# Kernel tuning notes

Measured on AMD Instinct MI355X. Metric: run time of the kernel, lower is better.

## Reference

```python
import jax, jax.numpy as jnp
import numpy as np

PATCH = 14

def _patchify(t, p):
    # (B,C,H,W) -> (B*pH*pW, C, p*p)
    B, C, H, W = t.shape
    pH, pW = H // p, W // p
    t = t.reshape(B, C, pH, p, pW, p).transpose(0, 2, 4, 1, 3, 5)
    return t.reshape(B * pH * pW, C, p * p)

def _unpatchify(t, B, C, H, W, p):
    pH, pW = H // p, W // p
    t = t.reshape(B, pH, pW, C, p, p).transpose(0, 3, 1, 4, 2, 5)
    return t.reshape(B, C, H, W)

def setup_inputs() -> dict:
    key = jax.random.key(0)
    ks = jax.random.split(key, 9)
    B, C, H, W = 4, 256, 224, 224
    s = 1.0 / np.sqrt(C)
    return {
        "x": jax.random.normal(ks[0], (B, C, H, W), jnp.float32),
        "skip0": jax.random.normal(ks[1], (B, C, 112, 112), jnp.float32),
        "skip1": jax.random.normal(ks[2], (B, C, 56, 56), jnp.float32),
        "Wq": jax.random.normal(ks[3], (C, C), jnp.float32) * s,
        "bq": jax.random.normal(ks[4], (C,), jnp.float32) * 0.01,
        "Wk": jax.random.normal(ks[5], (C, C), jnp.float32) * s,
        "bk": jax.random.normal(ks[6], (C,), jnp.float32) * 0.01,
        "Wv": jax.random.normal(ks[7], (C, C), jnp.float32) * s,
        "bv": jax.random.normal(ks[8], (C,), jnp.float32) * 0.01,
    }

def reference(x, skip0, skip1, Wq, bq, Wk, bk, Wv, bv):
    B, C, H, W = x.shape
    p = PATCH
    xp = _patchify(x, p)                       # (N, C, L), L = p*p
    # 1x1 conv on x (query) is shared across skips
    Q = jnp.einsum('oc,ncl->nol', Wq, xp) + bq[None, :, None]
    out = 0.0
    for skip in (skip0, skip1):
        sk = jax.image.resize(skip, (B, C, H, W), method='bilinear')  # align_corners=False
        sp = _patchify(sk, p)
        K = jnp.einsum('oc,ncl->nol', Wk, sp) + bk[None, :, None]
        V = jnp.einsum('oc,ncl->nol', Wv, sp) + bv[None, :, None]
        attn = jax.nn.softmax(jnp.einsum('ncl,ncm->nlm', Q, K), axis=-1)  # unscaled, per original
        out = out + jnp.einsum('nlm,ncm->ncl', attn, V)
    return _unpatchify(out, B, C, H, W, p)
```

## Files before the change

### kernel.cpp

```cpp
#include <hip/hip_runtime.h>

typedef _Float16 f16;
typedef _Float16 f16x8 __attribute__((ext_vector_type(8)));
typedef float f32x4 __attribute__((ext_vector_type(4)));

#define DEV static __device__ __forceinline__

constexpr int  NPATCH = 1024;
constexpr int  LLEN   = 196;
constexpr long NLROWS = (long)NPATCH * LLEN;

DEV void g2l16(const void* g, void* l) {
  __builtin_amdgcn_global_load_lds(
      (const __attribute__((address_space(1))) unsigned int*)g,
      (__attribute__((address_space(3))) unsigned int*)l, 16, 0, 0);
}

DEV unsigned pk2(float a, float b) {
  union { f16 h[2]; unsigned u; } z;
  z.h[0] = (f16)a; z.h[1] = (f16)b;
  return z.u;
}

__global__ __launch_bounds__(256) void k0_prep(
    const float* __restrict__ Wq, const float* __restrict__ Wk,
    const float* __restrict__ Wv, const float* __restrict__ bq,
    f16* __restrict__ G16, f16* __restrict__ Wv16, float* __restrict__ u32) {
  int bx = blockIdx.x, t = threadIdx.x;
  if (bx < 256) {
    int c = bx;
    float acc = 0.f;
    for (int o = 0; o < 256; ++o) acc += Wq[o*256 + c] * Wk[o*256 + t];
    G16[c*256 + t] = (f16)acc;
  } else if (bx == 256) {
    float acc = 0.f;
    for (int o = 0; o < 256; ++o) acc += bq[o] * Wk[o*256 + t];
    u32[t] = acc;
  } else {
    for (int r = 0; r < 256; ++r) Wv16[r*256 + t] = (f16)Wv[r*256 + t];
  }
}

__global__ __launch_bounds__(256) void k1_pack(
    const float* __restrict__ src, int Hs, int Ws, float invS,
    f16* __restrict__ dst, float* __restrict__ ub4,
    const float* __restrict__ u32, int do_ub) {
  __shared__ unsigned tile[32 * 225];
  __shared__ float us[64];
  int bx = blockIdx.x;
  int cc0 = (bx & 3) * 64;
  int bi = bx >> 2;
  int i  = bi % 14; bi /= 14;
  int py = bi & 15; int b = bi >> 4;
  int y = py*14 + i;
  int t = threadIdx.x;
  if (t < 64) us[t] = u32[cc0 + t];

  if (invS == 1.0f) {
    int xh = t & 7, pr = t >> 3;
    const float* b0 = src + ((long)(b*256 + cc0 + 2*pr)) * 50176 + y*224;
    const float* b1 = b0 + 50176;
#pragma unroll
    for (int it = 0; it < 7; ++it) {
      int x0 = (it*8 + xh) * 4;
      float4 va = *(const float4*)(b0 + x0);
      float4 vb = *(const float4*)(b1 + x0);
      tile[pr*225 + x0 + 0] = pk2(va.x, vb.x);
      tile[pr*225 + x0 + 1] = pk2(va.y, vb.y);
      tile[pr*225 + x0 + 2] = pk2(va.z, vb.z);
      tile[pr*225 + x0 + 3] = pk2(va.w, vb.w);
    }
  } else {
    float fy  = (y + 0.5f) * invS - 0.5f;
    float y0f = floorf(fy);
    float wy1 = fy - y0f, wy0 = 1.f - wy1;
    int y0 = (int)y0f, y1 = (int)y0f + 1;
    y0 = min(max(y0, 0), Hs-1); y1 = min(max(y1, 0), Hs-1);
    long plane = (long)Hs * Ws;
    int xl = t & 63, c4 = t >> 6;
    for (int xp = 0; xp < 4; ++xp) {
      int x = xp*64 + xl;
      if (x < 224) {
        float fx  = (x + 0.5f) * invS - 0.5f;
        float x0f = floorf(fx);
        float wx1 = fx - x0f, wx0 = 1.f - wx1;
        int x0 = (int)x0f, x1 = (int)x0f + 1;
        x0 = min(max(x0, 0), Ws-1); x1 = min(max(x1, 0), Ws-1);
        int o00 = y0*Ws + x0, o01 = y0*Ws + x1;
        int o10 = y1*Ws + x0, o11 = y1*Ws + x1;
#pragma unroll
        for (int pp = 0; pp < 8; ++pp) {
          int pr = c4*8 + pp;
          const float* base0 = src + ((long)(b*256 + cc0 + 2*pr)) * plane;
          const float* base1 = base0 + plane;
          float va = wy0*(wx0*base0[o00] + wx1*base0[o01])
                   + wy1*(wx0*base0[o10] + wx1*base0[o11]);
          float vb = wy0*(wx0*base1[o00] + wx1*base1[o01])
                   + wy1*(wx0*base1[o10] + wx1*base1[o11]);
          tile[pr*225 + x] = pk2(va, vb);
        }
      }
    }
  }
  __syncthreads();
  int q = t & 7, xg = t >> 3;
  float4 u0, u1;
  if (do_ub) {
    u0 = *(const float4*)(us + q*8);
    u1 = *(const float4*)(us + q*8 + 4);
  }
  for (int xo = 0; xo < 7; ++xo) {
    int x = xo*32 + xg;
    unsigned p0 = tile[(q*4+0)*225 + x];
    unsigned p1 = tile[(q*4+1)*225 + x];
    unsigned p2 = tile[(q*4+2)*225 + x];
    unsigned p3 = tile[(q*4+3)*225 + x];
    int px = x / 14, j = x % 14;
    int m = i*14 + j;
    long nm = (long)(b*256 + py*16 + px) * 196 + m;
    uint4 w; w.x = p0; w.y = p1; w.z = p2; w.w = p3;
    *reinterpret_cast<uint4*>(dst + nm*256 + cc0 + q*8) = w;
    if (do_ub) {
      union { unsigned u; f16 h[2]; } c0, c1, c2, c3;
      c0.u = p0; c1.u = p1; c2.u = p2; c3.u = p3;
      float part = u0.x*(float)c0.h[0] + u0.y*(float)c0.h[1]
                 + u0.z*(float)c1.h[0] + u0.w*(float)c1.h[1]
                 + u1.x*(float)c2.h[0] + u1.y*(float)c2.h[1]
                 + u1.z*(float)c3.h[0] + u1.w*(float)c3.h[1];
      part += __shfl_xor(part, 1);
      part += __shfl_xor(part, 2);
      part += __shfl_xor(part, 4);
      if (q == 0) ub4[(long)(bx & 3) * NLROWS + nm] = part;
    }
  }
}

__global__ __launch_bounds__(256) void k2_kv(
    const f16* __restrict__ SPT, const f16* __restrict__ G16,
    const f16* __restrict__ Wv16, f16* __restrict__ KtT, f16* __restrict__ VT2) {
  __shared__ __align__(16) char ldsA[64 * 80];
  __shared__ __align__(16) char ldsB[512 * 80];
  int tid = threadIdx.x;
  int lane = tid & 63, wv = tid >> 6;
  long nm0 = (long)blockIdx.x * 64;
  f32x4 zero = {0.f, 0.f, 0.f, 0.f};
  f32x4 acc[4][8];
#pragma unroll
  for (int a = 0; a < 4; ++a)
#pragma unroll
    for (int bb = 0; bb < 8; ++bb) acc[a][bb] = zero;
  int col0 = wv * 128;
  int r15 = lane & 15, quad = lane >> 4;
  for (int k0 = 0; k0 < 256; k0 += 32) {
    __syncthreads();
#pragma unroll
    for (int call = 0; call < 2; ++call) {
      int slot = call*256 + tid;
      if (slot < 320) {
        int row = slot / 5, part = slot % 5;
        int pp_ = part < 4 ? part : 0;
        g2l16(SPT + ((nm0 + row)*256 + k0 + pp_*8), ldsA + slot*16);
      }
    }
#pragma unroll
    for (int call = 0; call < 10; ++call) {
      int slot = call*256 + tid;
      int row = slot / 5, part = slot % 5;
      int pp_ = part < 4 ? part : 0;
      const f16* g = (row < 256) ? (G16 + (row*256 + k0 + pp_*8))
                                 : (Wv16 + ((row - 256)*256 + k0 + pp_*8));
      g2l16(g, ldsB + slot*16);
    }
    __syncthreads();
    f16x8 af[4];
#pragma unroll
    for (int rt = 0; rt < 4; ++rt)
      af[rt] = *(const f16x8*)(ldsA + (rt*16 + r15)*80 + quad*16);
#pragma unroll
    for (int tc = 0; tc < 8; ++tc) {
      f16x8 bf = *(const f16x8*)(ldsB + (col0 + tc*16 + r15)*80 + quad*16);
#pragma unroll
      for (int rt = 0; rt < 4; ++rt)
        acc[rt][tc] = __builtin_amdgcn_mfma_f32_16x16x32_f16(af[rt], bf, acc[rt][tc], 0, 0, 0);
    }
  }
  __syncthreads();
  f16* ldsV = (f16*)ldsB;
  if (wv >= 2) {
#pragma unroll
    for (int rt = 0; rt < 4; ++rt)
#pragma unroll
      for (int tc = 0; tc < 8; ++tc) {
        int o = col0 - 256 + tc*16 + r15;
#pragma unroll
        for (int reg = 0; reg < 4; ++reg) {
          int row = rt*16 + quad*4 + reg;
          ldsV[row*258 + o] = (f16)acc[rt][tc][reg];
        }
      }
  } else {
#pragma unroll
    for (int rt = 0; rt < 4; ++rt)
#pragma unroll
      for (int tc = 0; tc < 8; ++tc) {
        int colc = col0 + tc*16 + r15;
#pragma unroll
        for (int reg = 0; reg < 4; ++reg) {
          long row = nm0 + rt*16 + quad*4 + reg;
          KtT[row*256 + colc] = (f16)acc[rt][tc][reg];
        }
      }
  }
  __syncthreads();
  {
    int row = tid & 63;
    long nm = nm0 + row;
    int n = (int)(nm / 196), m = (int)(nm % 196);
    long vbase = ((long)n * 256) * 224 + m;
    int o0 = (tid >> 6) * 64;
    for (int it = 0; it < 64; ++it) {
      int o = o0 + it;
      VT2[vbase + (long)o * 224] = ldsV[row*258 + o];
    }
  }
}

__global__ __launch_bounds__(256) void k3_s(
    const f16* __restrict__ XT, const f16* __restrict__ KtT,
    const float* __restrict__ ub, f16* __restrict__ Pout) {
  __shared__ __align__(16) char ldsA[64 * 144];
  __shared__ __align__(16) char ldsB[208 * 144];
  __shared__ float ubs[208];
  int tid = threadIdx.x;
  int lane = tid & 63, wv = tid >> 6;
  int bx = blockIdx.x;
  int n  = ((bx >> 5) << 3) | (bx & 7);
  int l0 = ((bx >> 3) & 3) * 64;
  long base = (long)n * 196;
  for (int s = tid; s < 208; s += 256) {
    float v = 0.f;
    if (s < 196) {
      long o = base + s;
      v = ub[o] + ub[NLROWS + o] + ub[2*NLROWS + o] + ub[3*NLROWS + o];
    }
    ubs[s] = v;
  }
  f32x4 zero = {0.f, 0.f, 0.f, 0.f};
  f32x4 acc[13];
#pragma unroll
  for (int t = 0; t < 13; ++t) acc[t] = zero;
  int r15 = lane & 15, quad = lane >> 4;
  for (int k0 = 0; k0 < 256; k0 += 64) {
    __syncthreads();
#pragma unroll
    for (int call = 0; call < 3; ++call) {
      int slot = call*256 + tid;
      if (slot < 576) {
        int row = slot / 9, part = slot % 9;
        int pp_ = part < 8 ? part : 0;
        int l = l0 + row; l = l > 195 ? 195 : l;
        g2l16(XT + ((base + l)*256 + k0 + pp_*8), ldsA + slot*16);
      }
    }
#pragma unroll
    for (int call = 0; call < 8; ++call) {
      int slot = call*256 + tid;
      if (slot < 1872) {
        int row = slot / 9, part = slot % 9;
        int pp_ = part < 8 ? part : 0;
        int m = row > 195 ? 195 : row;
        g2l16(KtT + ((base + m)*256 + k0 + pp_*8), ldsB + slot*16);
      }
    }
    __syncthreads();
#pragma unroll
    for (int ks = 0; ks < 2; ++ks) {
      f16x8 af = *(const f16x8*)(ldsA + (wv*16 + r15)*144 + (ks*4 + quad)*16);
#pragma unroll
      for (int t = 0; t < 13; ++t) {
        f16x8 bf = *(const f16x8*)(ldsB + (t*16 + r15)*144 + (ks*4 + quad)*16);
        acc[t] = __builtin_amdgcn_mfma_f32_16x16x32_f16(af, bf, acc[t], 0, 0, 0);
      }
    }
  }
  float mx[4] = {-1e30f, -1e30f, -1e30f, -1e30f};
#pragma unroll
  for (int t = 0; t < 13; ++t) {
    int colb = t*16 + r15;
    float ubv = ubs[colb];
    bool valid = colb < 196;
#pragma unroll
    for (int reg = 0; reg < 4; ++reg) {
      float v = acc[t][reg] + ubv;
      acc[t][reg] = v;
      if (valid) mx[reg] = fmaxf(mx[reg], v);
    }
  }
#pragma unroll
  for (int reg = 0; reg < 4; ++reg) {
    float m = mx[reg];
    m = fmaxf(m, __shfl_xor(m, 1));
    m = fmaxf(m, __shfl_xor(m, 2));
    m = fmaxf(m, __shfl_xor(m, 4));
    m = fmaxf(m, __shfl_xor(m, 8));
    mx[reg] = m;
  }
  float sum[4] = {0.f, 0.f, 0.f, 0.f};
#pragma unroll
  for (int t = 0; t < 13; ++t) {
    int colb = t*16 + r15;
    bool valid = colb < 196;
#pragma unroll
    for (int reg = 0; reg < 4; ++reg) {
      float p = valid ? __expf(acc[t][reg] - mx[reg]) : 0.f;
      acc[t][reg] = p;
      sum[reg] += p;
    }
  }
#pragma unroll
  for (int reg = 0; reg < 4; ++reg) {
    float s = sum[reg];
    s += __shfl_xor(s, 1);
    s += __shfl_xor(s, 2);
    s += __shfl_xor(s, 4);
    s += __shfl_xor(s, 8);
    sum[reg] = 1.0f / s;
  }
#pragma unroll
  for (int reg = 0; reg < 4; ++reg) {
    int l = l0 + wv*16 + quad*4 + reg;
    if (l < 196) {
      long prow = (base + l) * 224;
#pragma unroll
      for (int t = 0; t < 13; ++t)
        Pout[prow + t*16 + r15] = (f16)(acc[t][reg] * sum[reg]);
      Pout[prow + 208 + r15] = (f16)0.f;
    }
  }
}

__global__ __launch_bounds__(256) void k4_o(
    const f16* __restrict__ Pbuf, const f16* __restrict__ VT2,
    f16* __restrict__ Obuf, int mode) {
  __shared__ __align__(16) char ldsA[2][64 * 80];
  __shared__ __align__(16) char ldsB[2][256 * 80];
  int tid = threadIdx.x;
  int lane = tid & 63, wv = tid >> 6;
  int bx = blockIdx.x;
  int n  = ((bx >> 5) << 3) | (bx & 7);
  int l0 = ((bx >> 3) & 3) * 64;
  f32x4 zero = {0.f, 0.f, 0.f, 0.f};
  f32x4 acc[16];
#pragma unroll
  for (int t = 0; t < 16; ++t) acc[t] = zero;
  int r15 = lane & 15, quad = lane >> 4;

  auto stage = [&](int buf, int m0) {
#pragma unroll
    for (int call = 0; call < 2; ++call) {
      int slot = call*256 + tid;
      if (slot < 320) {
        int row = slot / 5, part = slot % 5;
        int pp_ = part < 4 ? part : 0;
        long nl = (long)n*196 + l0 + row;
        if (nl > NLROWS - 1) nl = NLROWS - 1;
        g2l16(Pbuf + (nl*224 + m0 + pp_*8), ldsA[buf] + slot*16);
      }
    }
#pragma unroll
    for (int call = 0; call < 5; ++call) {
      int slot = call*256 + tid;
      int row = slot / 5, part = slot % 5;
      int pp_ = part < 4 ? part : 0;
      g2l16(VT2 + (((long)(n*256 + row))*224 + m0 + pp_*8), ldsB[buf] + slot*16);
    }
  };

  stage(0, 0);
  __syncthreads();
  for (int it = 0; it < 7; ++it) {
    int cur = it & 1;
    if (it < 6) stage(cur ^ 1, 32*(it+1));
    f16x8 af = *(const f16x8*)(ldsA[cur] + (wv*16 + r15)*80 + quad*16);
#pragma unroll
    for (int t = 0; t < 16; ++t) {
      f16x8 bf = *(const f16x8*)(ldsB[cur] + (t*16 + r15)*80 + quad*16);
      acc[t] = __builtin_amdgcn_mfma_f32_16x16x32_f16(af, bf, acc[t], 0, 0, 0);
    }
    __syncthreads();
  }
#pragma unroll
  for (int reg = 0; reg < 4; ++reg) {
    int l = l0 + wv*16 + quad*4 + reg;
    if (l < 196) {
      long orow = ((long)n*196 + l) * 256;
#pragma unroll
      for (int t = 0; t < 16; ++t) {
        int c = t*16 + r15;
        float v = acc[t][reg];
        if (mode == 0) Obuf[orow + c] = (f16)v;
        else           Obuf[orow + c] = (f16)(v + (float)Obuf[orow + c]);
      }
    }
  }
}

__global__ __launch_bounds__(256) void k5_unpatch(
    const f16* __restrict__ Obuf, const float* __restrict__ bv,
    float* __restrict__ out) {
  __shared__ float lds[64 * 225];
  int bx = blockIdx.x;
  int cc = (bx & 3) * 64;  bx >>= 2;
  int i  = bx % 14; bx /= 14;
  int py = bx & 15; int b = bx >> 4;
  int t = threadIdx.x;
  int cl = t & 63, pg = t >> 6;
  for (int it = 0; it < 56; ++it) {
    int pr = it*4 + pg;
    int px = pr / 14, j = pr % 14;
    int n = b*256 + py*16 + px;
    float v = (float)Obuf[((long)n*196 + i*14 + j)*256 + cc + cl];
    lds[cl*225 + px*14 + j] = v;
  }
  __syncthreads();
  int yy = py*14 + i;
  for (int c = 0; c < 64; ++c) {
    float bb = 2.0f * bv[cc + c];
    if (t < 224)
      out[(((long)(b*256 + cc + c))*224 + yy)*224 + t] = lds[c*225 + t] + bb;
  }
}

extern "C" void kernel_launch(void* const* d_in, const int* in_sizes, int n_in,
                              void* d_out, int out_size, void* d_ws, size_t ws_size,
                              hipStream_t stream) {
  (void)in_sizes; (void)n_in; (void)out_size; (void)ws_size;
  const float* x     = (const float*)d_in[0];
  const float* skip0 = (const float*)d_in[1];
  const float* skip1 = (const float*)d_in[2];
  const float* Wq    = (const float*)d_in[3];
  const float* bq    = (const float*)d_in[4];
  const float* Wk    = (const float*)d_in[5];
  const float* Wv    = (const float*)d_in[7];
  const float* bv    = (const float*)d_in[8];
  float* out = (float*)d_out;

  char* ws = (char*)d_ws;
  size_t off = 0;
  auto alloc = [&](size_t bytes) {
    char* p = ws + off;
    off += (bytes + 255) & ~(size_t)255;
    return p;
  };
  f16*   XT   = (f16*)  alloc((size_t)NLROWS * 256 * 2);
  f16*   SPT  = (f16*)  alloc((size_t)NLROWS * 256 * 2);
  f16*   KtT  = (f16*)  alloc((size_t)NLROWS * 256 * 2);
  f16*   VT2  = (f16*)  alloc((size_t)NPATCH * 256 * 224 * 2);
  f16*   Obuf = (f16*)  alloc((size_t)NLROWS * 256 * 2);
  float* ub   = (float*)alloc((size_t)NLROWS * 4 * 4);
  f16*   G16  = (f16*)  alloc(256 * 256 * 2);
  f16*   Wv16 = (f16*)  alloc(256 * 256 * 2);
  float* u32  = (float*)alloc(256 * 4);
  f16*   P    = SPT;

  k0_prep<<<258, 256, 0, stream>>>(Wq, Wk, Wv, bq, G16, Wv16, u32);
  k1_pack<<<3584, 256, 0, stream>>>(x, 224, 224, 1.0f, XT, nullptr, u32, 0);

  const float* skips[2] = {skip0, skip1};
  int   hs[2]   = {112, 56};
  float invs[2] = {0.5f, 0.25f};
  for (int s = 0; s < 2; ++s) {
    k1_pack<<<3584, 256, 0, stream>>>(skips[s], hs[s], hs[s], invs[s], SPT, ub, u32, 1);
    k2_kv<<<3136, 256, 0, stream>>>(SPT, G16, Wv16, KtT, VT2);
    k3_s <<<4096, 256, 0, stream>>>(XT, KtT, ub, P);
    k4_o <<<4096, 256, 0, stream>>>(P, VT2, Obuf, s);
  }
  k5_unpatch<<<3584, 256, 0, stream>>>(Obuf, bv, out);
}
```

Baseline: 1.709 ms.

## Fuse score-softmax and PV kernels to keep probabilities in LDS

Merges the attention-score/softmax kernel with the probability-times-V kernel, so the normalized probabilities are written to shared memory instead of a global P buffer and read straight back for the second GEMM. This removes a global write and read of the full probability matrix and one launch per skip. In exchange the K-loop step shrinks to 32, which doubles the barrier count. The V staging is now single-buffered with a barrier on every iteration, and the larger LDS footprint (about 50KB) may lower occupancy.

```diff
diff --git a/kernel.cpp b/kernel.cpp
--- a/kernel.cpp
+++ b/kernel.cpp
@@ -225,12 +225,15 @@
   }
 }
 
-__global__ __launch_bounds__(256) void k3_s(
+__global__ __launch_bounds__(256) void k3_sv(
     const f16* __restrict__ XT, const f16* __restrict__ KtT,
-    const float* __restrict__ ub, f16* __restrict__ Pout) {
-  __shared__ __align__(16) char ldsA[64 * 144];
-  __shared__ __align__(16) char ldsB[208 * 144];
+    const float* __restrict__ ub, const f16* __restrict__ VT2,
+    f16* __restrict__ Obuf, int mode) {
+  __shared__ __align__(16) char lds[50176];
   __shared__ float ubs[208];
+  char* ldsA = lds;
+  char* ldsB = lds + 5120;
+  char* ldsV = lds + 29696;
   int tid = threadIdx.x;
   int lane = tid & 63, wv = tid >> 6;
   int bx = blockIdx.x;
@@ -250,39 +253,47 @@
 #pragma unroll
   for (int t = 0; t < 13; ++t) acc[t] = zero;
   int r15 = lane & 15, quad = lane >> 4;
-  for (int k0 = 0; k0 < 256; k0 += 64) {
+  long vrow = ((long)(n*256)) * 224;
+
+  for (int k0 = 0; k0 < 256; k0 += 32) {
     __syncthreads();
 #pragma unroll
-    for (int call = 0; call < 3; ++call) {
+    for (int call = 0; call < 2; ++call) {
       int slot = call*256 + tid;
-      if (slot < 576) {
-        int row = slot / 9, part = slot % 9;
-        int pp_ = part < 8 ? part : 0;
+      if (slot < 320) {
+        int row = slot / 5, part = slot % 5;
+        int pp_ = part < 4 ? part : 0;
         int l = l0 + row; l = l > 195 ? 195 : l;
         g2l16(XT + ((base + l)*256 + k0 + pp_*8), ldsA + slot*16);
       }
     }
 #pragma unroll
-    for (int call = 0; call < 8; ++call) {
+    for (int call = 0; call < 5; ++call) {
       int slot = call*256 + tid;
-      if (slot < 1872) {
-        int row = slot / 9, part = slot % 9;
-        int pp_ = part < 8 ? part : 0;
+      if (slot < 1040) {
+        int row = slot / 5, part = slot % 5;
+        int pp_ = part < 8 ? (part < 4 ? part : 0) : 0;
         int m = row > 195 ? 195 : row;
         g2l16(KtT + ((base + m)*256 + k0 + pp_*8), ldsB + slot*16);
       }
     }
     __syncthreads();
-#pragma unroll
-    for (int ks = 0; ks < 2; ++ks) {
-      f16x8 af = *(const f16x8*)(ldsA + (wv*16 + r15)*144 + (ks*4 + quad)*16);
-#pragma unroll
-      for (int t = 0; t < 13; ++t) {
-        f16x8 bf = *(const f16x8*)(ldsB + (t*16 + r15)*144 + (ks*4 + quad)*16);
-        acc[t] = __builtin_amdgcn_mfma_f32_16x16x32_f16(af, bf, acc[t], 0, 0, 0);
-      }
-    }
-  }
+    f16x8 af = *(const f16x8*)(ldsA + (wv*16 + r15)*80 + quad*16);
+#pragma unroll
+    for (int t = 0; t < 13; ++t) {
+      f16x8 bf = *(const f16x8*)(ldsB + (t*16 + r15)*80 + quad*16);
+      acc[t] = __builtin_amdgcn_mfma_f32_16x16x32_f16(af, bf, acc[t], 0, 0, 0);
+    }
+  }
+
+#pragma unroll
+  for (int call = 0; call < 5; ++call) {
+    int slot = call*256 + tid;
+    int row = slot / 5, part = slot % 5;
+    int pp_ = part < 4 ? part : 0;
+    g2l16(VT2 + (vrow + (long)row*224 + pp_*8), ldsV + slot*16);
+  }
+
   float mx[4] = {-1e30f, -1e30f, -1e30f, -1e30f};
 #pragma unroll
   for (int t = 0; t < 13; ++t) {
@@ -326,78 +337,53 @@
     s += __shfl_xor(s, 8);
     sum[reg] = 1.0f / s;
   }
+
+  __syncthreads();
+#pragma unroll
+  for (int reg = 0; reg < 4; ++reg) {
+    int row = wv*16 + quad*4 + reg;
+    float sc = sum[reg];
+#pragma unroll
+    for (int t = 0; t < 13; ++t)
+      *(f16*)(lds + row*464 + (t*16 + r15)*2) = (f16)(acc[t][reg] * sc);
+  }
+  {
+    int row = tid >> 2, mq = tid & 3;
+    *(long*)(lds + row*464 + 416 + mq*8) = 0;
+  }
+
+  f32x4 oacc[16];
+#pragma unroll
+  for (int t = 0; t < 16; ++t) oacc[t] = zero;
+  for (int it = 0; it < 7; ++it) {
+    if (it > 0) {
+      __syncthreads();
+#pragma unroll
+      for (int call = 0; call < 5; ++call) {
+        int slot = call*256 + tid;
+        int row = slot / 5, part = slot % 5;
+        int pp_ = part < 4 ? part : 0;
+        g2l16(VT2 + (vrow + (long)row*224 + it*32 + pp_*8), ldsV + slot*16);
+      }
+    }
+    __syncthreads();
+    f16x8 af = *(const f16x8*)(lds + (wv*16 + r15)*464 + it*64 + quad*16);
+#pragma unroll
+    for (int t = 0; t < 16; ++t) {
+      f16x8 bf = *(const f16x8*)(ldsV + (t*16 + r15)*80 + quad*16);
+      oacc[t] = __builtin_amdgcn_mfma_f32_16x16x32_f16(af, bf, oacc[t], 0, 0, 0);
+    }
+  }
+
 #pragma unroll
   for (int reg = 0; reg < 4; ++reg) {
     int l = l0 + wv*16 + quad*4 + reg;
     if (l < 196) {
-      long prow = (base + l) * 224;
-#pragma unroll
-      for (int t = 0; t < 13; ++t)
-        Pout[prow + t*16 + r15] = (f16)(acc[t][reg] * sum[reg]);
-      Pout[prow + 208 + r15] = (f16)0.f;
-    }
-  }
-}
-
-__global__ __launch_bounds__(256) void k4_o(
-    const f16* __restrict__ Pbuf, const f16* __restrict__ VT2,
-    f16* __restrict__ Obuf, int mode) {
-  __shared__ __align__(16) char ldsA[2][64 * 80];
-  __shared__ __align__(16) char ldsB[2][256 * 80];
-  int tid = threadIdx.x;
-  int lane = tid & 63, wv = tid >> 6;
-  int bx = blockIdx.x;
-  int n  = ((bx >> 5) << 3) | (bx & 7);
-  int l0 = ((bx >> 3) & 3) * 64;
-  f32x4 zero = {0.f, 0.f, 0.f, 0.f};
-  f32x4 acc[16];
-#pragma unroll
-  for (int t = 0; t < 16; ++t) acc[t] = zero;
-  int r15 = lane & 15, quad = lane >> 4;
-
-  auto stage = [&](int buf, int m0) {
-#pragma unroll
-    for (int call = 0; call < 2; ++call) {
-      int slot = call*256 + tid;
-      if (slot < 320) {
-        int row = slot / 5, part = slot % 5;
-        int pp_ = part < 4 ? part : 0;
-        long nl = (long)n*196 + l0 + row;
-        if (nl > NLROWS - 1) nl = NLROWS - 1;
-        g2l16(Pbuf + (nl*224 + m0 + pp_*8), ldsA[buf] + slot*16);
-      }
-    }
-#pragma unroll
-    for (int call = 0; call < 5; ++call) {
-      int slot = call*256 + tid;
-      int row = slot / 5, part = slot % 5;
-      int pp_ = part < 4 ? part : 0;
-      g2l16(VT2 + (((long)(n*256 + row))*224 + m0 + pp_*8), ldsB[buf] + slot*16);
-    }
-  };
-
-  stage(0, 0);
-  __syncthreads();
-  for (int it = 0; it < 7; ++it) {
-    int cur = it & 1;
-    if (it < 6) stage(cur ^ 1, 32*(it+1));
-    f16x8 af = *(const f16x8*)(ldsA[cur] + (wv*16 + r15)*80 + quad*16);
-#pragma unroll
-    for (int t = 0; t < 16; ++t) {
-      f16x8 bf = *(const f16x8*)(ldsB[cur] + (t*16 + r15)*80 + quad*16);
-      acc[t] = __builtin_amdgcn_mfma_f32_16x16x32_f16(af, bf, acc[t], 0, 0, 0);
-    }
-    __syncthreads();
-  }
-#pragma unroll
-  for (int reg = 0; reg < 4; ++reg) {
-    int l = l0 + wv*16 + quad*4 + reg;
-    if (l < 196) {
-      long orow = ((long)n*196 + l) * 256;
+      long orow = (base + l) * 256;
 #pragma unroll
       for (int t = 0; t < 16; ++t) {
         int c = t*16 + r15;
-        float v = acc[t][reg];
+        float v = oacc[t][reg];
         if (mode == 0) Obuf[orow + c] = (f16)v;
         else           Obuf[orow + c] = (f16)(v + (float)Obuf[orow + c]);
       }
@@ -461,7 +447,6 @@
   f16*   G16  = (f16*)  alloc(256 * 256 * 2);
   f16*   Wv16 = (f16*)  alloc(256 * 256 * 2);
   float* u32  = (float*)alloc(256 * 4);
-  f16*   P    = SPT;
 
   k0_prep<<<258, 256, 0, stream>>>(Wq, Wk, Wv, bq, G16, Wv16, u32);
   k1_pack<<<3584, 256, 0, stream>>>(x, 224, 224, 1.0f, XT, nullptr, u32, 0);
@@ -472,8 +457,7 @@
   for (int s = 0; s < 2; ++s) {
     k1_pack<<<3584, 256, 0, stream>>>(skips[s], hs[s], hs[s], invs[s], SPT, ub, u32, 1);
     k2_kv<<<3136, 256, 0, stream>>>(SPT, G16, Wv16, KtT, VT2);
-    k3_s <<<4096, 256, 0, stream>>>(XT, KtT, ub, P);
-    k4_o <<<4096, 256, 0, stream>>>(P, VT2, Obuf, s);
+    k3_sv<<<4096, 256, 0, stream>>>(XT, KtT, ub, VT2, Obuf, s);
   }
   k5_unpatch<<<3584, 256, 0, stream>>>(Obuf, bv, out);
 }
```

Result: faster. 1.556 ms (-8.9%).
